# Kernel tuning notes

Measured on AMD Instinct MI355X. Metric: run time of the kernel, lower is better.

## Reference

```python
import jax, jax.numpy as jnp
import numpy as np

B = 16384          # batch size
S = 7              # grid size (hard-coded in original)
IMG = 448.0        # image size (hard-coded)
CELL = IMG / S     # 64.0 pixels per cell
LAMBDA_COORD = 5.0
LAMBDA_NOOBJ = 0.5


def setup_inputs() -> dict:
    key = jax.random.key(0)
    k1, k2, k3 = jax.random.split(key, 3)
    # predictions: raw head output [B, 30, 7, 7]; keep >= 0.05 so sqrt(w), sqrt(h) are safe
    input_ = jax.random.uniform(k1, (B, 30, S, S), jnp.float32, 0.05, 1.0)
    # targets already channels-last [B, 7, 7, 30]
    target = jax.random.uniform(k2, (B, S, S, 30), jnp.float32, 0.05, 1.0)
    # objectness channel must be exactly 1.0 where an object exists (code tests == 1)
    conf = (jax.random.uniform(k3, (B, S, S)) < 0.25).astype(jnp.float32)
    target = target.at[..., 4].set(conf)
    return {"input_": input_, "target": target}


def _grid_offsets(dtype):
    # flattened [B*49] pixel offsets of each cell's top-left corner
    g = jnp.arange(S, dtype=dtype)
    gx = jnp.broadcast_to(g[None, :], (S, S)).reshape(-1) * CELL  # varies with column
    gy = jnp.broadcast_to(g[:, None], (S, S)).reshape(-1) * CELL  # varies with row
    return jnp.tile(gx, B), jnp.tile(gy, B)


def _decode_box(p, c, gx, gy):
    # p: [N,30]; box at columns c..c+4 -> clamped corner coords in pixels
    cx = p[:, c] * CELL + gx
    cy = p[:, c + 1] * CELL + gy
    w = p[:, c + 2] * IMG
    h = p[:, c + 3] * IMG
    x1 = jnp.clip(cx - w * 0.5, 0.0, IMG)
    y1 = jnp.clip(cy - h * 0.5, 0.0, IMG)
    x2 = jnp.clip(cx + w * 0.5, 0.0, IMG)
    y2 = jnp.clip(cy + h * 0.5, 0.0, IMG)
    return x1, y1, x2, y2


def _iou(a, b):
    ax1, ay1, ax2, ay2 = a
    bx1, by1, bx2, by2 = b
    l = jnp.maximum(ax1, bx1)
    r = jnp.minimum(ax2, bx2)
    t = jnp.maximum(ay1, by1)
    bo = jnp.minimum(ay2, by2)
    m = (l < r) & (t < bo)
    inter = (r - l) * (bo - t)
    union = (ax2 - ax1) * (ay2 - ay1) + (bx2 - bx1) * (by2 - by1)
    denom = union - inter
    return jnp.where(m, inter / jnp.where(m, denom, 1.0), 0.0)


def _yolo_loss(input_, target):
    # [B,30,7,7] -> [B,7,7,30] -> [N,30]
    x = jnp.transpose(input_, (0, 2, 3, 1)).reshape(-1, 30)
    t = target.reshape(-1, 30)
    gx, gy = _grid_offsets(x.dtype)

    iou1 = _iou(_decode_box(x, 0, gx, gy), _decode_box(t, 0, gx, gy))
    iou2 = _iou(_decode_box(x, 5, gx, gy), _decode_box(t, 5, gx, gy))
    mask = iou1 < iou2                      # True -> second predicted box is responsible
    iou = jnp.where(mask, iou2, iou1)

    sel = jnp.where(mask[:, None], x[:, 5:10], x[:, :5])  # responsible box [N,5]
    w = (t[:, 4] == 1.0).astype(x.dtype)                   # hasObj as 0/1 weights

    coord = jnp.sum(w * ((sel[:, 0] - t[:, 0]) ** 2 + (sel[:, 1] - t[:, 1]) ** 2))
    size = jnp.sum(w * ((jnp.sqrt(sel[:, 2]) - jnp.sqrt(t[:, 2])) ** 2
                        + (jnp.sqrt(sel[:, 3]) - jnp.sqrt(t[:, 3])) ** 2))
    conf = jnp.sum(w * (sel[:, 4] - iou) ** 2)
    noobj = jnp.sum((1.0 - w) * sel[:, 4] ** 2)
    cls = jnp.sum(w[:, None] * (x[:, 10:] - t[:, 10:]) ** 2)

    return (LAMBDA_COORD * coord + LAMBDA_COORD * size + conf
            + LAMBDA_NOOBJ * noobj + cls)


def reference(input_, target):
    return _yolo_loss(input_, target)
```

## Files before the change

### kernel.cpp

```cpp
#include <hip/hip_runtime.h>


#define NCH   30
#define CELLS 49
#define TPB   256
#define IMGSZ 448.0f
#define CELLSZ 64.0f

__device__ __forceinline__ float iou_f(float ax1, float ay1, float ax2, float ay2,
                                       float bx1, float by1, float bx2, float by2) {
    float l  = fmaxf(ax1, bx1);
    float r  = fminf(ax2, bx2);
    float t  = fmaxf(ay1, by1);
    float bo = fminf(ay2, by2);
    bool  m  = (l < r) && (t < bo);
    float inter = (r - l) * (bo - t);
    float uni   = (ax2 - ax1) * (ay2 - ay1) + (bx2 - bx1) * (by2 - by1);
    float denom = uni - inter;
    return m ? (inter / denom) : 0.0f;
}

__device__ __forceinline__ void decode_box(float p0, float p1, float p2, float p3,
                                           float gx, float gy,
                                           float& x1, float& y1, float& x2, float& y2) {
    float cx = p0 * CELLSZ + gx;
    float cy = p1 * CELLSZ + gy;
    float w  = p2 * IMGSZ;
    float h  = p3 * IMGSZ;
    x1 = fminf(fmaxf(cx - w * 0.5f, 0.0f), IMGSZ);
    y1 = fminf(fmaxf(cy - h * 0.5f, 0.0f), IMGSZ);
    x2 = fminf(fmaxf(cx + w * 0.5f, 0.0f), IMGSZ);
    y2 = fminf(fmaxf(cy + h * 0.5f, 0.0f), IMGSZ);
}

__global__ __launch_bounds__(TPB) void yolo_loss_kernel(
        const float* __restrict__ input,
        const float* __restrict__ target,
        float* __restrict__ out,
        int ncells) {
    __shared__ float red[TPB / 64];

    const int tid = threadIdx.x;
    const int n   = blockIdx.x * TPB + tid;

    float loss = 0.0f;
    if (n < ncells) {
        const float2* __restrict__ tp = reinterpret_cast<const float2*>(target) + (long long)n * 15;
        float2 tv[15];
        #pragma unroll
        for (int k = 0; k < 15; ++k) tv[k] = tp[k];

        const int b    = n / CELLS;
        const int cell = n - b * CELLS;
        const float* __restrict__ ip = input + b * (NCH * CELLS) + cell;
        float x[NCH];
        #pragma unroll
        for (int c = 0; c < NCH; ++c) x[c] = ip[c * CELLS];

        float tl[NCH];
        #pragma unroll
        for (int k = 0; k < 15; ++k) { tl[2 * k] = tv[k].x; tl[2 * k + 1] = tv[k].y; }

        const int row  = cell / 7;
        const int col  = cell - row * 7;
        const float gx = (float)col * CELLSZ;
        const float gy = (float)row * CELLSZ;

        float p0x1, p0y1, p0x2, p0y2, p1x1, p1y1, p1x2, p1y2;
        decode_box(x[0], x[1], x[2], x[3], gx, gy, p0x1, p0y1, p0x2, p0y2);
        decode_box(x[5], x[6], x[7], x[8], gx, gy, p1x1, p1y1, p1x2, p1y2);
        float t0x1, t0y1, t0x2, t0y2, t1x1, t1y1, t1x2, t1y2;
        decode_box(tl[0], tl[1], tl[2], tl[3], gx, gy, t0x1, t0y1, t0x2, t0y2);
        decode_box(tl[5], tl[6], tl[7], tl[8], gx, gy, t1x1, t1y1, t1x2, t1y2);

        float iou1 = iou_f(p0x1, p0y1, p0x2, p0y2, t0x1, t0y1, t0x2, t0y2);
        float iou2 = iou_f(p1x1, p1y1, p1x2, p1y2, t1x1, t1y1, t1x2, t1y2);

        bool  mask = iou1 < iou2;
        float iou  = mask ? iou2 : iou1;
        float s0 = mask ? x[5] : x[0];
        float s1 = mask ? x[6] : x[1];
        float s2 = mask ? x[7] : x[2];
        float s3 = mask ? x[8] : x[3];
        float s4 = mask ? x[9] : x[4];

        float w = (tl[4] == 1.0f) ? 1.0f : 0.0f;

        float d0 = s0 - tl[0];
        float d1 = s1 - tl[1];
        float coord = d0 * d0 + d1 * d1;

        float ds2 = sqrtf(s2) - sqrtf(tl[2]);
        float ds3 = sqrtf(s3) - sqrtf(tl[3]);
        float size = ds2 * ds2 + ds3 * ds3;

        float dc = s4 - iou;
        float conf = dc * dc;
        float noobj = s4 * s4;

        float cls = 0.0f;
        #pragma unroll
        for (int c = 10; c < NCH; ++c) {
            float d = x[c] - tl[c];
            cls += d * d;
        }

        loss = w * (5.0f * (coord + size) + conf + cls) + 0.5f * (1.0f - w) * noobj;
    }

    #pragma unroll
    for (int off = 32; off > 0; off >>= 1)
        loss += __shfl_down(loss, off, 64);

    const int wid  = tid >> 6;
    const int lane = tid & 63;
    if (lane == 0) red[wid] = loss;
    __syncthreads();
    if (tid == 0) {
        float s = 0.0f;
        #pragma unroll
        for (int i = 0; i < TPB / 64; ++i) s += red[i];
        atomicAdd(out, s);
    }
}

extern "C" void kernel_launch(void* const* d_in, const int* in_sizes, int n_in,
                              void* d_out, int out_size, void* d_ws, size_t ws_size,
                              hipStream_t stream) {
    const float* input  = (const float*)d_in[0];
    const float* target = (const float*)d_in[1];
    float* out = (float*)d_out;

    const int ncells = in_sizes[0] / NCH;
    const int blocks = (ncells + TPB - 1) / TPB;

    hipMemsetAsync(d_out, 0, sizeof(float), stream);
    yolo_loss_kernel<<<blocks, TPB, 0, stream>>>(input, target, out, ncells);
}
```

Before: 207.3 us.

## Stage per-block batches into LDS via global_load_lds before computing loss

Each block now handles six whole batch items. It copies their input and target data into shared memory with direct global-to-LDS 16-byte loads, then computes every cell's loss from LDS. This replaces strided per-thread global reads (channel stride of 49 floats for input, 120-byte rows for target) with fully coalesced bulk loads. The cost is about 70KB of LDS per block, which limits occupancy, and LDS bank conflicts on the strided reads from shared memory.

```diff
diff --git a/kernel.cpp b/kernel.cpp
--- a/kernel.cpp
+++ b/kernel.cpp
@@ -1,11 +1,15 @@
 #include <hip/hip_runtime.h>
 
 
-#define NCH   30
-#define CELLS 49
-#define TPB   256
-#define IMGSZ 448.0f
-#define CELLSZ 64.0f
+#define NCH     30
+#define CELLS   49
+#define TPB     256
+#define WB      6
+#define BATCH_F 1470
+#define STAGE_F (WB * BATCH_F)
+#define STAGE_CHUNKS (STAGE_F / 4)
+#define IMGSZ   448.0f
+#define CELLSZ  64.0f
 
 __device__ __forceinline__ float iou_f(float ax1, float ay1, float ax2, float ay2,
                                        float bx1, float by1, float bx2, float by2) {
@@ -37,34 +41,50 @@
         const float* __restrict__ input,
         const float* __restrict__ target,
         float* __restrict__ out,
-        int ncells) {
+        int nbatch) {
+    __shared__ __align__(16) float s_in[STAGE_F];
+    __shared__ __align__(16) float s_tg[STAGE_F];
     __shared__ float red[TPB / 64];
 
     const int tid = threadIdx.x;
-    const int n   = blockIdx.x * TPB + tid;
+    const int b0  = blockIdx.x * WB;
+    const int nb  = min(WB, nbatch - b0);
+    const int nchunks = (nb * BATCH_F) >> 2;
 
+    const float* gin = input  + (long long)b0 * BATCH_F;
+    const float* gtg = target + (long long)b0 * BATCH_F;
+    #pragma unroll
+    for (int k = 0; k < (STAGE_CHUNKS + TPB - 1) / TPB; ++k) {
+        int i = k * TPB + tid;
+        if (i < nchunks) {
+            __builtin_amdgcn_global_load_lds(
+                (const __attribute__((address_space(1))) unsigned int*)(gin + i * 4),
+                (__attribute__((address_space(3))) unsigned int*)(&s_in[i * 4]),
+                16, 0, 0);
+            __builtin_amdgcn_global_load_lds(
+                (const __attribute__((address_space(1))) unsigned int*)(gtg + i * 4),
+                (__attribute__((address_space(3))) unsigned int*)(&s_tg[i * 4]),
+                16, 0, 0);
+        }
+    }
+    __syncthreads();
+
+    const int ncell = nb * CELLS;
     float loss = 0.0f;
-    if (n < ncells) {
-        const float2* __restrict__ tp = reinterpret_cast<const float2*>(target) + (long long)n * 15;
-        float2 tv[15];
-        #pragma unroll
-        for (int k = 0; k < 15; ++k) tv[k] = tp[k];
+    for (int local = tid; local < ncell; local += TPB) {
+        const int bb  = local / CELLS;
+        const int s   = local - bb * CELLS;
+        const int row = s / 7;
+        const int col = s - row * 7;
+        const float gx = (float)col * CELLSZ;
+        const float gy = (float)row * CELLSZ;
 
-        const int b    = n / CELLS;
-        const int cell = n - b * CELLS;
-        const float* __restrict__ ip = input + b * (NCH * CELLS) + cell;
+        const float* __restrict__ tl = &s_tg[local * NCH];
+        const float* __restrict__ ipx = &s_in[bb * BATCH_F + s];
+
         float x[NCH];
         #pragma unroll
-        for (int c = 0; c < NCH; ++c) x[c] = ip[c * CELLS];
-
-        float tl[NCH];
-        #pragma unroll
-        for (int k = 0; k < 15; ++k) { tl[2 * k] = tv[k].x; tl[2 * k + 1] = tv[k].y; }
-
-        const int row  = cell / 7;
-        const int col  = cell - row * 7;
-        const float gx = (float)col * CELLSZ;
-        const float gy = (float)row * CELLSZ;
+        for (int c = 0; c < NCH; ++c) x[c] = ipx[c * CELLS];
 
         float p0x1, p0y1, p0x2, p0y2, p1x1, p1y1, p1x2, p1y2;
         decode_box(x[0], x[1], x[2], x[3], gx, gy, p0x1, p0y1, p0x2, p0y2);
@@ -105,7 +125,7 @@
             cls += d * d;
         }
 
-        loss = w * (5.0f * (coord + size) + conf + cls) + 0.5f * (1.0f - w) * noobj;
+        loss += w * (5.0f * (coord + size) + conf + cls) + 0.5f * (1.0f - w) * noobj;
     }
 
     #pragma unroll
@@ -117,10 +137,10 @@
     if (lane == 0) red[wid] = loss;
     __syncthreads();
     if (tid == 0) {
-        float s = 0.0f;
+        float sum = 0.0f;
         #pragma unroll
-        for (int i = 0; i < TPB / 64; ++i) s += red[i];
-        atomicAdd(out, s);
+        for (int i = 0; i < TPB / 64; ++i) sum += red[i];
+        atomicAdd(out, sum);
     }
 }
 
@@ -131,9 +151,9 @@
     const float* target = (const float*)d_in[1];
     float* out = (float*)d_out;
 
-    const int ncells = in_sizes[0] / NCH;
-    const int blocks = (ncells + TPB - 1) / TPB;
+    const int nbatch = in_sizes[0] / BATCH_F;
+    const int blocks = (nbatch + WB - 1) / WB;
 
     hipMemsetAsync(d_out, 0, sizeof(float), stream);
-    yolo_loss_kernel<<<blocks, TPB, 0, stream>>>(input, target, out, ncells);
+    yolo_loss_kernel<<<blocks, TPB, 0, stream>>>(input, target, out, nbatch);
 }
```

Measured after the change: 205.6 us. About the same (-0.8%).
